# Kernel tuning notes

Measured on AMD Instinct MI355X. Metric: run time of the kernel, lower is better.

Reference implementation:

```python
import jax, jax.numpy as jnp
import numpy as np

N_NODES, N_EDGES, WIDTH = 50000, 640000, 128


def setup_inputs() -> dict:
    key = jax.random.key(0)
    k1, k2, k3 = jax.random.split(key, 3)
    x = jax.random.normal(k1, (N_NODES, WIDTH), dtype=jnp.float32)
    e = jax.random.randint(k2, (2, N_EDGES), 0, N_NODES, dtype=jnp.int32)
    # LinearBlock(2*width, width): Linear(256 -> 128) + ReLU
    W = jax.random.normal(k3, (WIDTH, 2 * WIDTH), dtype=jnp.float32) * (1.0 / np.sqrt(2 * WIDTH))
    b = jnp.zeros((WIDTH,), dtype=jnp.float32)
    return {"x": x, "e": e, "W": W, "b": b}


def reference(x, e, W, b):
    src, dst = e[0], e[1]
    # gather-subtract: diffs[k] = x[dst_k] - x[src_k]  -> [E, width]
    diffs = x[dst] - x[src]
    n = x.shape[0]
    # scatter_max over destination nodes; torch_scatter leaves empty segments at 0
    maxes = jax.ops.segment_max(diffs, dst, num_segments=n)  # [N, width]
    deg = jax.ops.segment_sum(jnp.ones((dst.shape[0],), jnp.float32), dst, num_segments=n)
    maxes = jnp.where((deg > 0)[:, None], maxes, 0.0)
    # LinearBlock (Linear + ReLU) on concat, then residual
    h = jnp.concatenate([x, maxes], axis=1)  # [N, 2*width]
    return x + jax.nn.relu(h @ W.T + b)
```

## Files before the change

kernel.cpp:

```cpp
#include <hip/hip_runtime.h>
#include <hip/hip_bf16.h>

#define WIDTH   128
#define NNODES  50000
#define NEDGES  640000
#define NTILES  3125
#define WLDS_STRIDE 264

#define RBLK    32
#define SSEG    8
#define RSZ     1563
#define SEG_I4  20000
#define C0      16
#define CAPB    128

#define BIN_BLOCKS  (RBLK * SSEG)
#define CVT_BLOCKS  1563
#define GRID_PREP   (BIN_BLOCKS + CVT_BLOCKS + 1)

typedef __attribute__((ext_vector_type(8))) short  short8;
typedef __attribute__((ext_vector_type(4))) short  short4_t;
typedef __attribute__((ext_vector_type(4))) float  float4_t;

__device__ inline short f2bf(float f) {
    union { float f; unsigned int u; } a;
    a.f = f;
    unsigned int r = a.u + 0x7FFFu + ((a.u >> 16) & 1u);
    return (short)(r >> 16);
}
__device__ inline unsigned int pack2bf(float a, float b) {
    unsigned int lo = (unsigned short)f2bf(a);
    unsigned int hi = (unsigned short)f2bf(b);
    return lo | (hi << 16);
}
__device__ inline float bflo(unsigned int u) { return __uint_as_float(u << 16); }
__device__ inline float bfhi(unsigned int u) { return __uint_as_float(u & 0xFFFF0000u); }

__global__ __launch_bounds__(1024) void prep_kernel(
    const float* __restrict__ x, const int* __restrict__ e,
    const float* __restrict__ W,
    uint2* __restrict__ xb2, uint2* __restrict__ wb2,
    int* __restrict__ counts2, int* __restrict__ buckets)
{
    __shared__ int cnt[RSZ];
    const int bid = blockIdx.x;
    const int tid = threadIdx.x;

    if (bid < BIN_BLOCKS) {
        int r = bid & (RBLK - 1);
        int s = bid >> 5;
        int base = r * RSZ;
        int rsz  = NNODES - base; if (rsz > RSZ) rsz = RSZ;

        for (int i = tid; i < RSZ; i += 1024) cnt[i] = 0;
        __syncthreads();

        const int4* dst4 = (const int4*)(e + NEDGES + s * (SEG_I4 * 4));
        const int4* src4 = (const int4*)(e + s * (SEG_I4 * 4));

        int i = tid;
        int4 d = (i < SEG_I4) ? dst4[i] : make_int4(-1, -1, -1, -1);
        while (i < SEG_I4) {
            int inx = i + 1024;
            int4 dn = d;
            if (inx < SEG_I4) dn = dst4[inx];

            unsigned a0 = (unsigned)(d.x - base);
            unsigned a1 = (unsigned)(d.y - base);
            unsigned a2 = (unsigned)(d.z - base);
            unsigned a3 = (unsigned)(d.w - base);
            bool m0 = a0 < (unsigned)rsz;
            bool m1 = a1 < (unsigned)rsz;
            bool m2 = a2 < (unsigned)rsz;
            bool m3 = a3 < (unsigned)rsz;
            if (m0 | m1 | m2 | m3) {
                int4 sv = src4[i];
                if (m0) { int p = atomicAdd(&cnt[a0], 1); if (p < C0) buckets[d.x * CAPB + s * C0 + p] = sv.x; }
                if (m1) { int p = atomicAdd(&cnt[a1], 1); if (p < C0) buckets[d.y * CAPB + s * C0 + p] = sv.y; }
                if (m2) { int p = atomicAdd(&cnt[a2], 1); if (p < C0) buckets[d.z * CAPB + s * C0 + p] = sv.z; }
                if (m3) { int p = atomicAdd(&cnt[a3], 1); if (p < C0) buckets[d.w * CAPB + s * C0 + p] = sv.w; }
            }
            d = dn; i = inx;
        }
        __syncthreads();
        for (int i2 = tid; i2 < rsz; i2 += 1024) {
            int c = cnt[i2]; if (c > C0) c = C0;
            counts2[(base + i2) * SSEG + s] = c;
        }
    } else if (bid < BIN_BLOCKS + CVT_BLOCKS) {
        int i = (bid - BIN_BLOCKS) * 1024 + tid;
        if (i < 1600000) {
            float4 v = ((const float4*)x)[i];
            uint2 p; p.x = pack2bf(v.x, v.y); p.y = pack2bf(v.z, v.w);
            xb2[i] = p;
        }
    } else {
        for (int j = tid; j < 8192; j += 1024) {
            float4 v = ((const float4*)W)[j];
            uint2 p; p.x = pack2bf(v.x, v.y); p.y = pack2bf(v.z, v.w);
            wb2[j] = p;
        }
    }
}

__global__ __launch_bounds__(256) void gather_min_bf16_kernel(
    const uint2* __restrict__ xb2, const int* __restrict__ counts2,
    const int* __restrict__ buckets, uint2* __restrict__ maxes2)
{
    int wave = (blockIdx.x * 256 + threadIdx.x) >> 6;
    int lane = threadIdx.x & 63;
    if (wave >= NNODES) return;
    int node = wave;

    int s0 = lane >> 4;
    int j  = lane & 15;
    int c0 = counts2[node * SSEG + s0];
    int c1 = counts2[node * SSEG + 4 + s0];
    int idx0 = buckets[node * CAPB + lane];
    int idx1 = buckets[node * CAPB + 64 + lane];
    bool v0 = j < c0;
    bool v1 = j < c1;
    unsigned long long m0 = __ballot(v0);
    unsigned long long m1 = __ballot(v1);
    int p0 = __builtin_amdgcn_mbcnt_hi((unsigned)(m0 >> 32),
             __builtin_amdgcn_mbcnt_lo((unsigned)m0, 0));
    int popc0 = __popcll(m0);
    int p1 = popc0 + __builtin_amdgcn_mbcnt_hi((unsigned)(m1 >> 32),
                     __builtin_amdgcn_mbcnt_lo((unsigned)m1, 0));
    int deg = popc0 + __popcll(m1);
    int t0 = v0 ? p0 : 63;
    int t1 = v1 ? p1 : 63;
    int r0 = __builtin_amdgcn_ds_permute(t0 << 2, idx0);
    int r1 = __builtin_amdgcn_ds_permute(t1 << 2, idx1);
    int myidx = (lane < popc0) ? r0 : r1;

    int h  = lane >> 5;
    int cl = lane & 31;

    float4 m; m.x = 3.4e38f; m.y = 3.4e38f; m.z = 3.4e38f; m.w = 3.4e38f;
#pragma unroll 1
    for (int j0 = 0; j0 < deg; j0 += 16) {
        uint2 v[8];
#pragma unroll
        for (int u = 0; u < 8; ++u) {
            int jc = j0 + 2 * u + h;
            jc = jc < deg ? jc : deg - 1;
            int src = __shfl(myidx, jc);
            v[u] = xb2[(size_t)src * 32 + cl];
        }
#pragma unroll
        for (int u = 0; u < 8; ++u) {
            m.x = fminf(m.x, bflo(v[u].x));
            m.y = fminf(m.y, bfhi(v[u].x));
            m.z = fminf(m.z, bflo(v[u].y));
            m.w = fminf(m.w, bfhi(v[u].y));
        }
    }
    m.x = fminf(m.x, __shfl_xor(m.x, 32));
    m.y = fminf(m.y, __shfl_xor(m.y, 32));
    m.z = fminf(m.z, __shfl_xor(m.z, 32));
    m.w = fminf(m.w, __shfl_xor(m.w, 32));

    if (h == 0) {
        uint2 o;
        if (deg > 0) {
            uint2 xv = xb2[(size_t)node * 32 + cl];
            o.x = pack2bf(bflo(xv.x) - m.x, bfhi(xv.x) - m.y);
            o.y = pack2bf(bflo(xv.y) - m.z, bfhi(xv.y) - m.w);
        } else {
            o.x = 0u; o.y = 0u;
        }
        maxes2[(size_t)node * 32 + cl] = o;
    }
}

__global__ __launch_bounds__(256) void fill_kernel(
    const int* __restrict__ e, int* __restrict__ counts, int* __restrict__ buckets)
{
    int i = blockIdx.x * 256 + threadIdx.x;
    if (i >= NEDGES) return;
    int src = e[i];
    int dst = e[NEDGES + i];
    int pos = atomicAdd(&counts[dst], 1);
    if (pos < 64) buckets[dst * 64 + pos] = src;
}

__global__ __launch_bounds__(256) void gather_min_fp32_kernel(
    const float* __restrict__ x, const int* __restrict__ counts,
    const int* __restrict__ buckets, unsigned int* __restrict__ maxes_u32)
{
    int wave = (blockIdx.x * 256 + threadIdx.x) >> 6;
    int lane = threadIdx.x & 63;
    if (wave >= NNODES) return;
    int node = wave;
    int deg  = counts[node];
    deg = deg > 64 ? 64 : deg;

    int myidx = (lane < deg) ? buckets[node * 64 + lane] : 0;
    int c = lane * 2;
    float2 m; m.x = 3.4e38f; m.y = 3.4e38f;
#pragma unroll 1
    for (int j0 = 0; j0 < deg; j0 += 8) {
        float2 v[8];
#pragma unroll
        for (int u = 0; u < 8; ++u) {
            int jc = j0 + u;
            jc = jc < deg ? jc : deg - 1;
            int src = __shfl(myidx, jc);
            v[u] = *(const float2*)(x + (size_t)src * WIDTH + c);
        }
#pragma unroll
        for (int u = 0; u < 8; ++u) {
            m.x = fminf(m.x, v[u].x);
            m.y = fminf(m.y, v[u].y);
        }
    }
    float2 o;
    if (deg > 0) {
        float2 xv = *(const float2*)(x + (size_t)node * WIDTH + c);
        o.x = xv.x - m.x;
        o.y = xv.y - m.y;
    } else { o.x = 0.f; o.y = 0.f; }
    maxes_u32[(size_t)node * 64 + lane] = pack2bf(o.x, o.y);
}

template<bool FAST>
__global__ __launch_bounds__(256, 2) void fused_gemm_kernel(
    const float* __restrict__ x, const short* __restrict__ xb,
    const short* __restrict__ maxes,
    const float* __restrict__ W, const short* __restrict__ Wb,
    const float* __restrict__ b, float* __restrict__ out)
{
    __shared__ short Wlds[WIDTH * WLDS_STRIDE];

    const int t = threadIdx.x;

    if (FAST) {
#pragma unroll
        for (int i = 0; i < 32; ++i) {
            int idx8 = t + i * 256;
            int flat = idx8 << 3;
            short8 w = *(const short8*)(Wb + flat);
            int n = flat >> 8;
            int k = flat & 255;
            *(short4_t*)&Wlds[n * WLDS_STRIDE + k]     = *(short4_t*)&w;
            *(short4_t*)&Wlds[n * WLDS_STRIDE + k + 4] = *((short4_t*)&w + 1);
        }
    } else {
#pragma unroll
        for (int i = 0; i < 32; ++i) {
            int idx4 = t + i * 256;
            int flat = idx4 << 2;
            float4 w = *(const float4*)(W + flat);
            int n = flat >> 8;
            int k = flat & 255;
            short4_t s;
            s.x = f2bf(w.x); s.y = f2bf(w.y); s.z = f2bf(w.z); s.w = f2bf(w.w);
            *(short4_t*)&Wlds[n * WLDS_STRIDE + k] = s;
        }
    }
    __syncthreads();

    const int wave  = t >> 6;
    const int lane  = t & 63;
    const int lm    = lane & 15;
    const int quad  = lane >> 4;
    const int nhalf = wave & 1;
    const int wpair = wave >> 1;
    const int ncol_base = nhalf * 64;

    short8 bfrag[4][8];
#pragma unroll
    for (int nt = 0; nt < 4; ++nt) {
        int n = ncol_base + nt * 16 + lm;
#pragma unroll
        for (int kt = 0; kt < 8; ++kt) {
            int k = kt * 32 + quad * 8;
            bfrag[nt][kt] = *(const short8*)&Wlds[n * WLDS_STRIDE + k];
        }
    }

    const int stride = gridDim.x * 2;
#pragma unroll 1
    for (int tile = blockIdx.x * 2 + wpair; tile < NTILES; tile += stride) {
        int row = tile * 16 + lm;
        const float* xr  = x     + (size_t)row * WIDTH;
        const short* xbr = FAST ? (xb + (size_t)row * WIDTH) : nullptr;
        const short* mr  = maxes + (size_t)row * WIDTH;

        float4_t acc[4];
#pragma unroll
        for (int nt = 0; nt < 4; ++nt) { acc[nt].x = 0.f; acc[nt].y = 0.f; acc[nt].z = 0.f; acc[nt].w = 0.f; }

#pragma unroll
        for (int kt = 0; kt < 8; ++kt) {
            int k = kt * 32 + quad * 8;
            short8 afrag;
            if (k < WIDTH) {
                if (FAST) {
                    afrag = *(const short8*)(xbr + k);
                } else {
                    float4 v0 = *(const float4*)(xr + k);
                    float4 v1 = *(const float4*)(xr + k + 4);
                    afrag[0] = f2bf(v0.x); afrag[1] = f2bf(v0.y);
                    afrag[2] = f2bf(v0.z); afrag[3] = f2bf(v0.w);
                    afrag[4] = f2bf(v1.x); afrag[5] = f2bf(v1.y);
                    afrag[6] = f2bf(v1.z); afrag[7] = f2bf(v1.w);
                }
            } else {
                afrag = *(const short8*)(mr + (k - WIDTH));
            }
#pragma unroll
            for (int nt = 0; nt < 4; ++nt) {
                acc[nt] = __builtin_amdgcn_mfma_f32_16x16x32_bf16(
                    afrag, bfrag[nt][kt], acc[nt], 0, 0, 0);
            }
        }

#pragma unroll
        for (int nt = 0; nt < 4; ++nt) {
            int col = ncol_base + nt * 16 + lm;
            float bias = b[col];
#pragma unroll
            for (int r = 0; r < 4; ++r) {
                int orow = tile * 16 + quad * 4 + r;
                float v = acc[nt][r] + bias;
                v = v > 0.f ? v : 0.f;
                size_t off = (size_t)orow * WIDTH + col;
                out[off] = x[off] + v;
            }
        }
    }
}

extern "C" void kernel_launch(void* const* d_in, const int* in_sizes, int n_in,
                              void* d_out, int out_size, void* d_ws, size_t ws_size,
                              hipStream_t stream) {
    const float* x = (const float*)d_in[0];
    const int*   e = (const int*)  d_in[1];
    const float* W = (const float*)d_in[2];
    const float* b = (const float*)d_in[3];
    float* out = (float*)d_out;

    char* ws = (char*)d_ws;

    const size_t off_buckets = 1600512;
    const size_t off_maxes   = off_buckets + 25600000;
    const size_t off_xb      = off_maxes + 12800000;
    const size_t off_wb      = off_xb + 12800000;
    const size_t need        = off_wb + 65536;

    if (ws_size >= need) {
        int*          counts2 = (int*)ws;
        int*          buckets = (int*)(ws + off_buckets);
        unsigned int* maxes   = (unsigned int*)(ws + off_maxes);
        short*        xb      = (short*)(ws + off_xb);
        short*        wb      = (short*)(ws + off_wb);

        prep_kernel<<<GRID_PREP, 1024, 0, stream>>>(
            x, e, W, (uint2*)xb, (uint2*)wb, counts2, buckets);
        gather_min_bf16_kernel<<<(NNODES + 3) / 4, 256, 0, stream>>>(
            (const uint2*)xb, counts2, buckets, (uint2*)maxes);
        fused_gemm_kernel<true><<<512, 256, 0, stream>>>(
            x, xb, (const short*)maxes, W, wb, b, out);
    } else {
        int*          counts  = (int*)ws;
        int*          buckets = (int*)(ws + 262144);
        unsigned int* maxes   = (unsigned int*)(ws + 262144 + 12800000);

        hipMemsetAsync(counts, 0, 262144, stream);
        fill_kernel<<<(NEDGES + 255) / 256, 256, 0, stream>>>(e, counts, buckets);
        gather_min_fp32_kernel<<<(NNODES + 3) / 4, 256, 0, stream>>>(
            x, counts, buckets, maxes);
        fused_gemm_kernel<false><<<512, 256, 0, stream>>>(
            x, nullptr, (const short*)maxes, W, nullptr, b, out);
    }
}
```

Baseline: 144.8 us.

## Split bf16 features into column quarters and gather per quarter with grid barrier

Stores bf16 x and the min-aggregate in four column-quarter planes so each gather pass touches a 3.2 MB slice that can stay cache-resident. Compacts bucket indices to 16-bit and counts to bytes to cut index traffic. The gather kernel becomes persistent, with 13 nodes per wave, and sweeps the quarters separated by a spin-based grid barrier. The GEMM reads its A fragments from the quarter layout. The barrier assumes all 1024 blocks are co-resident and gives up after a fixed iteration count. The 16-bit indices only hold because node ids stay below 65536.

```diff
diff --git a/kernel.cpp b/kernel.cpp
--- a/kernel.cpp
+++ b/kernel.cpp
@@ -15,8 +15,14 @@
 #define CAPB    128
 
 #define BIN_BLOCKS  (RBLK * SSEG)
-#define CVT_BLOCKS  1563
+#define CVT_BLOCKS  782
 #define GRID_PREP   (BIN_BLOCKS + CVT_BLOCKS + 1)
+
+#define QSZ_B   3200000
+#define QSZ_U   800000
+
+#define GQ_BLOCKS 1024
+#define NPW 13
 
 typedef __attribute__((ext_vector_type(8))) short  short8;
 typedef __attribute__((ext_vector_type(4))) short  short4_t;
@@ -39,8 +45,10 @@
 __global__ __launch_bounds__(1024) void prep_kernel(
     const float* __restrict__ x, const int* __restrict__ e,
     const float* __restrict__ W,
-    uint2* __restrict__ xb2, uint2* __restrict__ wb2,
-    int* __restrict__ counts2, int* __restrict__ buckets)
+    char* __restrict__ xbq, uint2* __restrict__ wb2,
+    unsigned char* __restrict__ counts8,
+    unsigned short* __restrict__ bucketsU,
+    int* __restrict__ bar)
 {
     __shared__ int cnt[RSZ];
     const int bid = blockIdx.x;
@@ -75,24 +83,33 @@
             bool m3 = a3 < (unsigned)rsz;
             if (m0 | m1 | m2 | m3) {
                 int4 sv = src4[i];
-                if (m0) { int p = atomicAdd(&cnt[a0], 1); if (p < C0) buckets[d.x * CAPB + s * C0 + p] = sv.x; }
-                if (m1) { int p = atomicAdd(&cnt[a1], 1); if (p < C0) buckets[d.y * CAPB + s * C0 + p] = sv.y; }
-                if (m2) { int p = atomicAdd(&cnt[a2], 1); if (p < C0) buckets[d.z * CAPB + s * C0 + p] = sv.z; }
-                if (m3) { int p = atomicAdd(&cnt[a3], 1); if (p < C0) buckets[d.w * CAPB + s * C0 + p] = sv.w; }
+                if (m0) { int p = atomicAdd(&cnt[a0], 1); if (p < C0) bucketsU[(size_t)d.x * CAPB + s * C0 + p] = (unsigned short)sv.x; }
+                if (m1) { int p = atomicAdd(&cnt[a1], 1); if (p < C0) bucketsU[(size_t)d.y * CAPB + s * C0 + p] = (unsigned short)sv.y; }
+                if (m2) { int p = atomicAdd(&cnt[a2], 1); if (p < C0) bucketsU[(size_t)d.z * CAPB + s * C0 + p] = (unsigned short)sv.z; }
+                if (m3) { int p = atomicAdd(&cnt[a3], 1); if (p < C0) bucketsU[(size_t)d.w * CAPB + s * C0 + p] = (unsigned short)sv.w; }
             }
             d = dn; i = inx;
         }
         __syncthreads();
         for (int i2 = tid; i2 < rsz; i2 += 1024) {
             int c = cnt[i2]; if (c > C0) c = C0;
-            counts2[(base + i2) * SSEG + s] = c;
+            counts8[(size_t)(base + i2) * SSEG + s] = (unsigned char)c;
         }
     } else if (bid < BIN_BLOCKS + CVT_BLOCKS) {
         int i = (bid - BIN_BLOCKS) * 1024 + tid;
-        if (i < 1600000) {
-            float4 v = ((const float4*)x)[i];
-            uint2 p; p.x = pack2bf(v.x, v.y); p.y = pack2bf(v.z, v.w);
-            xb2[i] = p;
+        if (i < 800000) {
+            const float4* xf = (const float4*)x;
+            float4 v0 = xf[2 * i];
+            float4 v1 = xf[2 * i + 1];
+            int f = i << 3;
+            int row = f >> 7;
+            int col = f & 127;
+            int q = col >> 5;
+            int chunk = (col & 31) >> 3;
+            uint4 p;
+            p.x = pack2bf(v0.x, v0.y); p.y = pack2bf(v0.z, v0.w);
+            p.z = pack2bf(v1.x, v1.y); p.w = pack2bf(v1.z, v1.w);
+            *(uint4*)(xbq + (size_t)q * QSZ_B + (size_t)row * 64 + chunk * 16) = p;
         }
     } else {
         for (int j = tid; j < 8192; j += 1024) {
@@ -100,77 +117,106 @@
             uint2 p; p.x = pack2bf(v.x, v.y); p.y = pack2bf(v.z, v.w);
             wb2[j] = p;
         }
-    }
-}
-
-__global__ __launch_bounds__(256) void gather_min_bf16_kernel(
-    const uint2* __restrict__ xb2, const int* __restrict__ counts2,
-    const int* __restrict__ buckets, uint2* __restrict__ maxes2)
+        if (tid < 4) bar[tid] = 0;
+    }
+}
+
+__global__ __launch_bounds__(256, 4) void gather_min_q_kernel(
+    const unsigned int* __restrict__ xbq,
+    const unsigned char* __restrict__ counts8,
+    const unsigned int* __restrict__ bucketsU32,
+    unsigned int* __restrict__ maxesq,
+    int* __restrict__ bar)
 {
-    int wave = (blockIdx.x * 256 + threadIdx.x) >> 6;
-    int lane = threadIdx.x & 63;
-    if (wave >= NNODES) return;
-    int node = wave;
-
-    int s0 = lane >> 4;
-    int j  = lane & 15;
-    int c0 = counts2[node * SSEG + s0];
-    int c1 = counts2[node * SSEG + 4 + s0];
-    int idx0 = buckets[node * CAPB + lane];
-    int idx1 = buckets[node * CAPB + 64 + lane];
-    bool v0 = j < c0;
-    bool v1 = j < c1;
-    unsigned long long m0 = __ballot(v0);
-    unsigned long long m1 = __ballot(v1);
-    int p0 = __builtin_amdgcn_mbcnt_hi((unsigned)(m0 >> 32),
-             __builtin_amdgcn_mbcnt_lo((unsigned)m0, 0));
-    int popc0 = __popcll(m0);
-    int p1 = popc0 + __builtin_amdgcn_mbcnt_hi((unsigned)(m1 >> 32),
-                     __builtin_amdgcn_mbcnt_lo((unsigned)m1, 0));
-    int deg = popc0 + __popcll(m1);
-    int t0 = v0 ? p0 : 63;
-    int t1 = v1 ? p1 : 63;
-    int r0 = __builtin_amdgcn_ds_permute(t0 << 2, idx0);
-    int r1 = __builtin_amdgcn_ds_permute(t1 << 2, idx1);
-    int myidx = (lane < popc0) ? r0 : r1;
-
-    int h  = lane >> 5;
-    int cl = lane & 31;
-
-    float4 m; m.x = 3.4e38f; m.y = 3.4e38f; m.z = 3.4e38f; m.w = 3.4e38f;
+    const int lane = threadIdx.x & 63;
+    const int gw   = blockIdx.x * 4 + (threadIdx.x >> 6);
+    const int base = gw * NPW;
+
+    const int gb = lane >> 3;
+    const int jj = (lane & 7) * 2;
+    const int ge = lane >> 4;
+    const int c  = lane & 15;
+
+    int myidx[NPW];
+    int deg[NPW];
+#pragma unroll
+    for (int t = 0; t < NPW; ++t) {
+        int node = base + t;
+        deg[t] = 0; myidx[t] = 0;
+        if (node < NNODES) {
+            uint2 cc = *(const uint2*)(counts8 + (size_t)node * 8);
+            unsigned int u = bucketsU32[(size_t)node * 64 + lane];
+            unsigned int cg = ((gb < 4 ? cc.x : cc.y) >> ((gb & 3) * 8)) & 0xFFu;
+            bool va = (unsigned)jj < cg;
+            bool vb = (unsigned)(jj + 1) < cg;
+            unsigned long long ma = __ballot(va);
+            unsigned long long mb = __ballot(vb);
+            int popcA = __popcll(ma);
+            int pA = __builtin_amdgcn_mbcnt_hi((unsigned)(ma >> 32),
+                      __builtin_amdgcn_mbcnt_lo((unsigned)ma, 0));
+            int pB = popcA + __builtin_amdgcn_mbcnt_hi((unsigned)(mb >> 32),
+                      __builtin_amdgcn_mbcnt_lo((unsigned)mb, 0));
+            int rA = __builtin_amdgcn_ds_permute((va ? pA : 63) << 2,
+                                                 (int)(u & 0xFFFFu));
+            int rB = __builtin_amdgcn_ds_permute(((vb && pB < 64) ? pB : 63) << 2,
+                                                 (int)(u >> 16));
+            deg[t]   = popcA + __popcll(mb);
+            myidx[t] = (lane < popcA) ? rA : rB;
+        }
+    }
+
 #pragma unroll 1
-    for (int j0 = 0; j0 < deg; j0 += 16) {
-        uint2 v[8];
-#pragma unroll
-        for (int u = 0; u < 8; ++u) {
-            int jc = j0 + 2 * u + h;
-            jc = jc < deg ? jc : deg - 1;
-            int src = __shfl(myidx, jc);
-            v[u] = xb2[(size_t)src * 32 + cl];
-        }
-#pragma unroll
-        for (int u = 0; u < 8; ++u) {
-            m.x = fminf(m.x, bflo(v[u].x));
-            m.y = fminf(m.y, bfhi(v[u].x));
-            m.z = fminf(m.z, bflo(v[u].y));
-            m.w = fminf(m.w, bfhi(v[u].y));
-        }
-    }
-    m.x = fminf(m.x, __shfl_xor(m.x, 32));
-    m.y = fminf(m.y, __shfl_xor(m.y, 32));
-    m.z = fminf(m.z, __shfl_xor(m.z, 32));
-    m.w = fminf(m.w, __shfl_xor(m.w, 32));
-
-    if (h == 0) {
-        uint2 o;
-        if (deg > 0) {
-            uint2 xv = xb2[(size_t)node * 32 + cl];
-            o.x = pack2bf(bflo(xv.x) - m.x, bfhi(xv.x) - m.y);
-            o.y = pack2bf(bflo(xv.y) - m.z, bfhi(xv.y) - m.w);
-        } else {
-            o.x = 0u; o.y = 0u;
-        }
-        maxes2[(size_t)node * 32 + cl] = o;
+    for (int q = 0; q < 4; ++q) {
+        const unsigned int* xq = xbq + (size_t)q * QSZ_U;
+        unsigned int* mq = maxesq + (size_t)q * QSZ_U;
+#pragma unroll
+        for (int t = 0; t < NPW; ++t) {
+            int node = base + t;
+            if (node < NNODES) {
+                int dg = deg[t];
+                float mlo = 3.4e38f, mhi = 3.4e38f;
+#pragma unroll 1
+                for (int j0 = 0; j0 < dg; j0 += 16) {
+                    unsigned int v[4];
+#pragma unroll
+                    for (int u = 0; u < 4; ++u) {
+                        int jc = j0 + u * 4 + ge;
+                        jc = jc < dg ? jc : dg - 1;
+                        int src = __shfl(myidx[t], jc);
+                        v[u] = xq[(size_t)src * 16 + c];
+                    }
+#pragma unroll
+                    for (int u = 0; u < 4; ++u) {
+                        mlo = fminf(mlo, bflo(v[u]));
+                        mhi = fminf(mhi, bfhi(v[u]));
+                    }
+                }
+                mlo = fminf(mlo, __shfl_xor(mlo, 16));
+                mhi = fminf(mhi, __shfl_xor(mhi, 16));
+                mlo = fminf(mlo, __shfl_xor(mlo, 32));
+                mhi = fminf(mhi, __shfl_xor(mhi, 32));
+                if (lane < 16) {
+                    unsigned int o = 0u;
+                    if (dg > 0) {
+                        unsigned int xv = xq[(size_t)node * 16 + lane];
+                        o = pack2bf(bflo(xv) - mlo, bfhi(xv) - mhi);
+                    }
+                    mq[(size_t)node * 16 + lane] = o;
+                }
+            }
+        }
+        if (q < 3) {
+            __syncthreads();
+            if (threadIdx.x == 0) {
+                __hip_atomic_fetch_add(&bar[q], 1, __ATOMIC_RELAXED,
+                                       __HIP_MEMORY_SCOPE_AGENT);
+                int it = 0;
+                while (__hip_atomic_load(&bar[q], __ATOMIC_RELAXED,
+                                         __HIP_MEMORY_SCOPE_AGENT) < GQ_BLOCKS
+                       && it < 20000) { ++it; __builtin_amdgcn_s_sleep(2); }
+            }
+            __syncthreads();
+        }
     }
 }
 
@@ -284,9 +330,9 @@
 #pragma unroll 1
     for (int tile = blockIdx.x * 2 + wpair; tile < NTILES; tile += stride) {
         int row = tile * 16 + lm;
-        const float* xr  = x     + (size_t)row * WIDTH;
-        const short* xbr = FAST ? (xb + (size_t)row * WIDTH) : nullptr;
-        const short* mr  = maxes + (size_t)row * WIDTH;
+        int ro  = row * 64 + quad * 16;
+        const float* xr = x     + (size_t)row * WIDTH;
+        const short* mr = maxes + (size_t)row * WIDTH;
 
         float4_t acc[4];
 #pragma unroll
@@ -294,21 +340,23 @@
 
 #pragma unroll
         for (int kt = 0; kt < 8; ++kt) {
-            int k = kt * 32 + quad * 8;
             short8 afrag;
-            if (k < WIDTH) {
-                if (FAST) {
-                    afrag = *(const short8*)(xbr + k);
-                } else {
+            if (FAST) {
+                const char* ap = ((kt < 4) ? (const char*)xb : (const char*)maxes)
+                                 + (size_t)(kt & 3) * QSZ_B + ro;
+                afrag = *(const short8*)ap;
+            } else {
+                int k = kt * 32 + quad * 8;
+                if (k < WIDTH) {
                     float4 v0 = *(const float4*)(xr + k);
                     float4 v1 = *(const float4*)(xr + k + 4);
                     afrag[0] = f2bf(v0.x); afrag[1] = f2bf(v0.y);
                     afrag[2] = f2bf(v0.z); afrag[3] = f2bf(v0.w);
                     afrag[4] = f2bf(v1.x); afrag[5] = f2bf(v1.y);
                     afrag[6] = f2bf(v1.z); afrag[7] = f2bf(v1.w);
+                } else {
+                    afrag = *(const short8*)(mr + (k - WIDTH));
                 }
-            } else {
-                afrag = *(const short8*)(mr + (k - WIDTH));
             }
 #pragma unroll
             for (int nt = 0; nt < 4; ++nt) {
@@ -344,25 +392,28 @@
 
     char* ws = (char*)d_ws;
 
-    const size_t off_buckets = 1600512;
-    const size_t off_maxes   = off_buckets + 25600000;
-    const size_t off_xb      = off_maxes + 12800000;
-    const size_t off_wb      = off_xb + 12800000;
+    const size_t off_counts  = 64;
+    const size_t off_buckets = 400128;
+    const size_t off_xbq     = off_buckets + 12800000;
+    const size_t off_maxesq  = off_xbq + 12800000;
+    const size_t off_wb      = off_maxesq + 12800000;
     const size_t need        = off_wb + 65536;
 
     if (ws_size >= need) {
-        int*          counts2 = (int*)ws;
-        int*          buckets = (int*)(ws + off_buckets);
-        unsigned int* maxes   = (unsigned int*)(ws + off_maxes);
-        short*        xb      = (short*)(ws + off_xb);
-        short*        wb      = (short*)(ws + off_wb);
+        int*            bar      = (int*)ws;
+        unsigned char*  counts8  = (unsigned char*)(ws + off_counts);
+        unsigned short* bucketsU = (unsigned short*)(ws + off_buckets);
+        char*           xbq      = ws + off_xbq;
+        unsigned int*   maxesq   = (unsigned int*)(ws + off_maxesq);
+        short*          wb       = (short*)(ws + off_wb);
 
         prep_kernel<<<GRID_PREP, 1024, 0, stream>>>(
-            x, e, W, (uint2*)xb, (uint2*)wb, counts2, buckets);
-        gather_min_bf16_kernel<<<(NNODES + 3) / 4, 256, 0, stream>>>(
-            (const uint2*)xb, counts2, buckets, (uint2*)maxes);
+            x, e, W, xbq, (uint2*)wb, counts8, bucketsU, bar);
+        gather_min_q_kernel<<<GQ_BLOCKS, 256, 0, stream>>>(
+            (const unsigned int*)xbq, counts8, (const unsigned int*)bucketsU,
+            maxesq, bar);
         fused_gemm_kernel<true><<<512, 256, 0, stream>>>(
-            x, xb, (const short*)maxes, W, wb, b, out);
+            x, (const short*)xbq, (const short*)maxesq, W, wb, b, out);
     } else {
         int*          counts  = (int*)ws;
         int*          buckets = (int*)(ws + 262144);
```

Measured after the change: 453.7 us. +213.3%, slower.
